# Kernel tuning notes

Measured on AMD Instinct MI355X. Metric: run time of the kernel, lower is better.

The kernel has to match this reference:

```python
import jax, jax.numpy as jnp
import numpy as np

CODEBOOK_SIZE = 512
LATENT_DIM = 12
BATCH = 512
TOKENS = 256


def setup_inputs() -> dict:
    key = jax.random.key(0)
    k1, k2 = jax.random.split(key)
    x = jax.random.normal(k1, (BATCH, TOKENS, LATENT_DIM), dtype=jnp.float32)
    # nn.Embedding init: uniform(-1/K, 1/K)
    lim = 1.0 / CODEBOOK_SIZE
    codebook = jax.random.uniform(k2, (CODEBOOK_SIZE, LATENT_DIM), dtype=jnp.float32,
                                  minval=-lim, maxval=lim)
    return {"x": x, "codebook": codebook}


def reference(x, codebook):
    # same as for torch.cdist (sqrt is monotonic).
    x2 = jnp.sum(x * x, axis=-1, keepdims=True)            # [B, N, 1]
    w2 = jnp.sum(codebook * codebook, axis=-1)             # [K]
    xw = jnp.einsum('bnd,kd->bnk', x, codebook)            # [B, N, K]
    dist2 = x2 - 2.0 * xw + w2                             # [B, N, K]
    indices = jnp.argmin(dist2, axis=-1)                   # [B, N] int
    quantized = codebook[indices]                          # [B, N, D]

    codebook_loss = jnp.mean((quantized - jax.lax.stop_gradient(x)) ** 2)
    commitment_loss = 0.25 * jnp.mean((jax.lax.stop_gradient(quantized) - x) ** 2)
    quantize_loss = codebook_loss + commitment_loss

    # straight-through estimator
    quantized_st = x + jax.lax.stop_gradient(quantized - x)
    return quantized_st, indices, quantize_loss
```

## Files before the change

### kernel.cpp

```cpp
#include <hip/hip_runtime.h>
#include <math.h>

namespace {
constexpr int KCB   = 512;
constexpr int DIM   = 12;
constexpr int NTOK  = 512 * 256;
constexpr int QSIZE = NTOK * DIM;
constexpr int NSPLIT = 8;
constexpr int KCHUNK = KCB / NSPLIT;
constexpr int TPT    = 4;
constexpr int TOKS_PER_BLOCK = 64 * TPT;
constexpr int NBLK   = NTOK / TOKS_PER_BLOCK;
constexpr int WVEC_FLOATS = KCB * DIM;
constexpr int CB_FLOATS   = WVEC_FLOATS + KCB;
constexpr int CB_F4       = CB_FLOATS / 4;
constexpr int SMEM_U64    = 3333;
constexpr int PARTIALS_OFF = 8192;

__global__ __launch_bounds__(256) void pack_cb(const float* __restrict__ cb,
                                               float* __restrict__ ws) {
    int k = blockIdx.x * blockDim.x + threadIdx.x;
    if (k >= KCB) return;
    float w[DIM];
#pragma unroll
    for (int d = 0; d < DIM; ++d) w[d] = cb[k * DIM + d];
    float w2 = 0.f;
#pragma unroll
    for (int d = 0; d < DIM; ++d) w2 += w[d] * w[d];
#pragma unroll
    for (int d = 0; d < DIM; ++d) ws[k * DIM + d] = w[d];
    ws[WVEC_FLOATS + k] = w2;
}

__device__ inline float code_score(const float (&xv)[DIM], float x2,
                                   const float4& c0, const float4& c1,
                                   const float4& c2, float w2k) {
    float xw = 0.f;
    xw = fmaf(xv[0],  c0.x, xw);
    xw = fmaf(xv[1],  c0.y, xw);
    xw = fmaf(xv[2],  c0.z, xw);
    xw = fmaf(xv[3],  c0.w, xw);
    xw = fmaf(xv[4],  c1.x, xw);
    xw = fmaf(xv[5],  c1.y, xw);
    xw = fmaf(xv[6],  c1.z, xw);
    xw = fmaf(xv[7],  c1.w, xw);
    xw = fmaf(xv[8],  c2.x, xw);
    xw = fmaf(xv[9],  c2.y, xw);
    xw = fmaf(xv[10], c2.z, xw);
    xw = fmaf(xv[11], c2.w, xw);
    return fmaf(-2.f, xw, x2) + w2k;
}

__global__ __launch_bounds__(512, 2) void vq_main(const float* __restrict__ x,
                                                  const float* __restrict__ cb,
                                                  const float* __restrict__ pk,
                                                  float* __restrict__ out,
                                                  float* __restrict__ partials) {
    __shared__ unsigned long long smem[SMEM_U64];
    __shared__ float lred[TPT];
    float* lds = (float*)smem;
    const int tid  = threadIdx.x;
    const int lane = tid & 63;
    const int s = __builtin_amdgcn_readfirstlane(tid >> 6);
    const int tbase = blockIdx.x * TOKS_PER_BLOCK;

    {
        float4* l4 = (float4*)lds;
        const float4* g4 = (const float4*)pk;
        for (int i = tid; i < CB_F4; i += 512) l4[i] = g4[i];
    }

    float xs[TPT][DIM];
    float x2[TPT];
#pragma unroll
    for (int j = 0; j < TPT; ++j) {
        const float4* xp = (const float4*)(x + (size_t)(tbase + j * 64 + lane) * DIM);
        float4 a0 = xp[0], a1 = xp[1], a2 = xp[2];
        xs[j][0] = a0.x; xs[j][1] = a0.y; xs[j][2]  = a0.z; xs[j][3]  = a0.w;
        xs[j][4] = a1.x; xs[j][5] = a1.y; xs[j][6]  = a1.z; xs[j][7]  = a1.w;
        xs[j][8] = a2.x; xs[j][9] = a2.y; xs[j][10] = a2.z; xs[j][11] = a2.w;
        float t2 = 0.f;
#pragma unroll
        for (int d = 0; d < DIM; ++d) t2 = fmaf(xs[j][d], xs[j][d], t2);
        x2[j] = t2;
    }

    __syncthreads();

    float best[TPT];
    int   bi[TPT];
#pragma unroll
    for (int j = 0; j < TPT; ++j) { best[j] = INFINITY; bi[j] = 0; }

    const int k0 = s * KCHUNK;
    const float* w2v = lds + WVEC_FLOATS;

    float4 A0, A1, A2; float w2A;
    float4 B0, B1, B2; float w2B;
    {
        const float* c = lds + (size_t)k0 * DIM;
        A0 = *(const float4*)(c + 0);
        A1 = *(const float4*)(c + 4);
        A2 = *(const float4*)(c + 8);
        w2A = w2v[k0];
    }
#pragma unroll 4
    for (int kk = 0; kk < KCHUNK; kk += 2) {
        {
            const float* c = lds + (size_t)(k0 + kk + 1) * DIM;
            B0 = *(const float4*)(c + 0);
            B1 = *(const float4*)(c + 4);
            B2 = *(const float4*)(c + 8);
            w2B = w2v[k0 + kk + 1];
        }
        {
            const int k = k0 + kk;
#pragma unroll
            for (int j = 0; j < TPT; ++j) {
                float d = code_score(xs[j], x2[j], A0, A1, A2, w2A);
                bool c = d < best[j];
                best[j] = c ? d : best[j];
                bi[j]   = c ? k : bi[j];
            }
        }
        {
            const float* c = lds + (size_t)(k0 + kk + 2) * DIM;
            A0 = *(const float4*)(c + 0);
            A1 = *(const float4*)(c + 4);
            A2 = *(const float4*)(c + 8);
            w2A = w2v[k0 + kk + 2];
        }
        {
            const int k = k0 + kk + 1;
#pragma unroll
            for (int j = 0; j < TPT; ++j) {
                float d = code_score(xs[j], x2[j], B0, B1, B2, w2B);
                bool c = d < best[j];
                best[j] = c ? d : best[j];
                bi[j]   = c ? k : bi[j];
            }
        }
    }

    auto mkkey = [](float v, int k) {
        unsigned su = __float_as_uint(v);
        su = (su & 0x80000000u) ? ~su : (su | 0x80000000u);
        return ((unsigned long long)su << 32) | (unsigned)k;
    };
    __syncthreads();
#pragma unroll
    for (int j = 0; j < TPT; ++j)
        smem[s * TOKS_PER_BLOCK + j * 64 + lane] = mkkey(best[j], bi[j]);
    __syncthreads();

    if (s < TPT) {
        const int tok = s * 64 + lane;
        unsigned long long m = smem[tok];
#pragma unroll
        for (int r = 1; r < NSPLIT; ++r) {
            unsigned long long v = smem[r * TOKS_PER_BLOCK + tok];
            m = v < m ? v : m;
        }
        const int bid = (int)(m & 0xffffffffULL);
        unsigned eu = (unsigned)(m >> 32);
        unsigned orig = (eu & 0x80000000u) ? (eu ^ 0x80000000u) : ~eu;
        const float bsc = __uint_as_float(orig);
        const int t = tbase + tok;

        float xv[DIM];
#pragma unroll
        for (int j = 0; j < TPT; ++j)
            if (j == s) {
#pragma unroll
                for (int d = 0; d < DIM; ++d) xv[d] = xs[j][d];
            }

        const float4* wrow = (const float4*)(cb + (size_t)bid * DIM);
        float4 q0 = wrow[0], q1 = wrow[1], q2 = wrow[2];
        float qs[DIM] = {q0.x, q0.y, q0.z, q0.w, q1.x, q1.y, q1.z, q1.w,
                         q2.x, q2.y, q2.z, q2.w};

        float4* qo = (float4*)(out + (size_t)t * DIM);
        float4 r0, r1, r2;
        r0.x = xv[0] + (qs[0] - xv[0]);    r0.y = xv[1] + (qs[1] - xv[1]);
        r0.z = xv[2] + (qs[2] - xv[2]);    r0.w = xv[3] + (qs[3] - xv[3]);
        r1.x = xv[4] + (qs[4] - xv[4]);    r1.y = xv[5] + (qs[5] - xv[5]);
        r1.z = xv[6] + (qs[6] - xv[6]);    r1.w = xv[7] + (qs[7] - xv[7]);
        r2.x = xv[8] + (qs[8] - xv[8]);    r2.y = xv[9] + (qs[9] - xv[9]);
        r2.z = xv[10] + (qs[10] - xv[10]); r2.w = xv[11] + (qs[11] - xv[11]);
        qo[0] = r0; qo[1] = r1; qo[2] = r2;

        out[QSIZE + t] = (float)bid;

        float ls = bsc * (1.25f / (float)QSIZE);
#pragma unroll
        for (int off = 32; off > 0; off >>= 1) ls += __shfl_down(ls, off);
        if (lane == 0) lred[s] = ls;
    }
    __syncthreads();
    if (tid == 0)
        partials[blockIdx.x] = (lred[0] + lred[1]) + (lred[2] + lred[3]);
}

__global__ __launch_bounds__(512) void reduce_loss(const float* __restrict__ partials,
                                                   float* __restrict__ out) {
    __shared__ float r[8];
    float v = partials[threadIdx.x];
#pragma unroll
    for (int off = 32; off > 0; off >>= 1) v += __shfl_down(v, off);
    if ((threadIdx.x & 63) == 0) r[threadIdx.x >> 6] = v;
    __syncthreads();
    if (threadIdx.x == 0) {
        float t = 0.f;
#pragma unroll
        for (int i = 0; i < 8; ++i) t += r[i];
        out[QSIZE + NTOK] = t;
    }
}
}

extern "C" void kernel_launch(void* const* d_in, const int* in_sizes, int n_in,
                              void* d_out, int out_size, void* d_ws, size_t ws_size,
                              hipStream_t stream) {
    const float* x  = (const float*)d_in[0];
    const float* cb = (const float*)d_in[1];
    float* out = (float*)d_out;
    float* pk  = (float*)d_ws;
    float* partials = (float*)d_ws + PARTIALS_OFF;

    pack_cb<<<2, 256, 0, stream>>>(cb, pk);
    vq_main<<<NBLK, 512, 0, stream>>>(x, cb, pk, out, partials);
    reduce_loss<<<1, 512, 0, stream>>>(partials, out);
}
```

Measured before the change: 94.52 us.

## Split codebook across blocks and move emission to a separate kernel

The scan kernel now handles half the codebook per block, doubling the grid to 1024 blocks, and computes codebook norms in LDS instead of in a separate pack kernel. Each block writes per-token min keys to workspace, and a new emit kernel merges the two halves, writes outputs, and accumulates the loss with atomicAdd. This targets low occupancy and tail effects from only 512 blocks and removes two tiny launches. In exchange it adds global traffic for the keys and a second read of x, and the atomic loss sum makes its float rounding order nondeterministic.

```diff
diff --git a/kernel.cpp b/kernel.cpp
--- a/kernel.cpp
+++ b/kernel.cpp
@@ -7,30 +7,17 @@
 constexpr int NTOK  = 512 * 256;
 constexpr int QSIZE = NTOK * DIM;
 constexpr int NSPLIT = 8;
-constexpr int KCHUNK = KCB / NSPLIT;
+constexpr int KHALF  = 2;
+constexpr int KCODES = KCB / KHALF;
+constexpr int KCHUNK = KCODES / NSPLIT;
 constexpr int TPT    = 4;
 constexpr int TOKS_PER_BLOCK = 64 * TPT;
-constexpr int NBLK   = NTOK / TOKS_PER_BLOCK;
-constexpr int WVEC_FLOATS = KCB * DIM;
-constexpr int CB_FLOATS   = WVEC_FLOATS + KCB;
-constexpr int CB_F4       = CB_FLOATS / 4;
-constexpr int SMEM_U64    = 3333;
-constexpr int PARTIALS_OFF = 8192;
-
-__global__ __launch_bounds__(256) void pack_cb(const float* __restrict__ cb,
-                                               float* __restrict__ ws) {
-    int k = blockIdx.x * blockDim.x + threadIdx.x;
-    if (k >= KCB) return;
-    float w[DIM];
-#pragma unroll
-    for (int d = 0; d < DIM; ++d) w[d] = cb[k * DIM + d];
-    float w2 = 0.f;
-#pragma unroll
-    for (int d = 0; d < DIM; ++d) w2 += w[d] * w[d];
-#pragma unroll
-    for (int d = 0; d < DIM; ++d) ws[k * DIM + d] = w[d];
-    ws[WVEC_FLOATS + k] = w2;
-}
+constexpr int NTG    = NTOK / TOKS_PER_BLOCK;
+constexpr int NBLK1  = NTG * KHALF;
+constexpr int WVEC   = KCODES * DIM;
+constexpr int SMEM_U64 = NSPLIT * TOKS_PER_BLOCK;
+constexpr int EMIT_THREADS = 256;
+constexpr int NBLK2 = NTOK / EMIT_THREADS;
 
 __device__ inline float code_score(const float (&xv)[DIM], float x2,
                                    const float4& c0, const float4& c1,
@@ -51,23 +38,32 @@
     return fmaf(-2.f, xw, x2) + w2k;
 }
 
-__global__ __launch_bounds__(512, 2) void vq_main(const float* __restrict__ x,
+__device__ inline unsigned long long mkkey(float v, int k) {
+    unsigned su = __float_as_uint(v);
+    su = (su & 0x80000000u) ? ~su : (su | 0x80000000u);
+    return ((unsigned long long)su << 32) | (unsigned)k;
+}
+
+__global__ __launch_bounds__(512, 6) void vq_scan(const float* __restrict__ x,
                                                   const float* __restrict__ cb,
-                                                  const float* __restrict__ pk,
-                                                  float* __restrict__ out,
-                                                  float* __restrict__ partials) {
+                                                  unsigned long long* __restrict__ keys,
+                                                  float* __restrict__ out) {
     __shared__ unsigned long long smem[SMEM_U64];
-    __shared__ float lred[TPT];
     float* lds = (float*)smem;
     const int tid  = threadIdx.x;
     const int lane = tid & 63;
     const int s = __builtin_amdgcn_readfirstlane(tid >> 6);
-    const int tbase = blockIdx.x * TOKS_PER_BLOCK;
+    const int tg = blockIdx.x & (NTG - 1);
+    const int kh = blockIdx.x >> 9;
+    const int kbase = kh * KCODES;
+    const int tbase = tg * TOKS_PER_BLOCK;
+
+    if (blockIdx.x == 0 && tid == 0) out[QSIZE + NTOK] = 0.f;
 
     {
+        const float4* g4 = (const float4*)(cb + (size_t)kbase * DIM);
         float4* l4 = (float4*)lds;
-        const float4* g4 = (const float4*)pk;
-        for (int i = tid; i < CB_F4; i += 512) l4[i] = g4[i];
+        for (int i = tid; i < WVEC / 4; i += 512) l4[i] = g4[i];
     }
 
     float xs[TPT][DIM];
@@ -87,34 +83,44 @@
 
     __syncthreads();
 
+    if (tid < KCODES) {
+        const float* w = lds + (size_t)tid * DIM;
+        float w2 = 0.f;
+#pragma unroll
+        for (int d = 0; d < DIM; ++d) w2 = fmaf(w[d], w[d], w2);
+        lds[WVEC + tid] = w2;
+    }
+    __syncthreads();
+
     float best[TPT];
     int   bi[TPT];
 #pragma unroll
     for (int j = 0; j < TPT; ++j) { best[j] = INFINITY; bi[j] = 0; }
 
-    const int k0 = s * KCHUNK;
-    const float* w2v = lds + WVEC_FLOATS;
+    const int k0l = s * KCHUNK;
+    const int gk0 = kbase + k0l;
+    const float* w2v = lds + WVEC;
 
     float4 A0, A1, A2; float w2A;
     float4 B0, B1, B2; float w2B;
     {
-        const float* c = lds + (size_t)k0 * DIM;
+        const float* c = lds + (size_t)k0l * DIM;
         A0 = *(const float4*)(c + 0);
         A1 = *(const float4*)(c + 4);
         A2 = *(const float4*)(c + 8);
-        w2A = w2v[k0];
+        w2A = w2v[k0l];
     }
 #pragma unroll 4
     for (int kk = 0; kk < KCHUNK; kk += 2) {
         {
-            const float* c = lds + (size_t)(k0 + kk + 1) * DIM;
+            const float* c = lds + (size_t)(k0l + kk + 1) * DIM;
             B0 = *(const float4*)(c + 0);
             B1 = *(const float4*)(c + 4);
             B2 = *(const float4*)(c + 8);
-            w2B = w2v[k0 + kk + 1];
-        }
-        {
-            const int k = k0 + kk;
+            w2B = w2v[k0l + kk + 1];
+        }
+        {
+            const int k = gk0 + kk;
 #pragma unroll
             for (int j = 0; j < TPT; ++j) {
                 float d = code_score(xs[j], x2[j], A0, A1, A2, w2A);
@@ -124,14 +130,14 @@
             }
         }
         {
-            const float* c = lds + (size_t)(k0 + kk + 2) * DIM;
+            const float* c = lds + (size_t)(k0l + kk + 2) * DIM;
             A0 = *(const float4*)(c + 0);
             A1 = *(const float4*)(c + 4);
             A2 = *(const float4*)(c + 8);
-            w2A = w2v[k0 + kk + 2];
-        }
-        {
-            const int k = k0 + kk + 1;
+            w2A = w2v[k0l + kk + 2];
+        }
+        {
+            const int k = gk0 + kk + 1;
 #pragma unroll
             for (int j = 0; j < TPT; ++j) {
                 float d = code_score(xs[j], x2[j], B0, B1, B2, w2B);
@@ -142,11 +148,6 @@
         }
     }
 
-    auto mkkey = [](float v, int k) {
-        unsigned su = __float_as_uint(v);
-        su = (su & 0x80000000u) ? ~su : (su | 0x80000000u);
-        return ((unsigned long long)su << 32) | (unsigned)k;
-    };
     __syncthreads();
 #pragma unroll
     for (int j = 0; j < TPT; ++j)
@@ -161,60 +162,56 @@
             unsigned long long v = smem[r * TOKS_PER_BLOCK + tok];
             m = v < m ? v : m;
         }
-        const int bid = (int)(m & 0xffffffffULL);
-        unsigned eu = (unsigned)(m >> 32);
-        unsigned orig = (eu & 0x80000000u) ? (eu ^ 0x80000000u) : ~eu;
-        const float bsc = __uint_as_float(orig);
-        const int t = tbase + tok;
-
-        float xv[DIM];
-#pragma unroll
-        for (int j = 0; j < TPT; ++j)
-            if (j == s) {
-#pragma unroll
-                for (int d = 0; d < DIM; ++d) xv[d] = xs[j][d];
-            }
-
-        const float4* wrow = (const float4*)(cb + (size_t)bid * DIM);
-        float4 q0 = wrow[0], q1 = wrow[1], q2 = wrow[2];
-        float qs[DIM] = {q0.x, q0.y, q0.z, q0.w, q1.x, q1.y, q1.z, q1.w,
-                         q2.x, q2.y, q2.z, q2.w};
-
-        float4* qo = (float4*)(out + (size_t)t * DIM);
-        float4 r0, r1, r2;
-        r0.x = xv[0] + (qs[0] - xv[0]);    r0.y = xv[1] + (qs[1] - xv[1]);
-        r0.z = xv[2] + (qs[2] - xv[2]);    r0.w = xv[3] + (qs[3] - xv[3]);
-        r1.x = xv[4] + (qs[4] - xv[4]);    r1.y = xv[5] + (qs[5] - xv[5]);
-        r1.z = xv[6] + (qs[6] - xv[6]);    r1.w = xv[7] + (qs[7] - xv[7]);
-        r2.x = xv[8] + (qs[8] - xv[8]);    r2.y = xv[9] + (qs[9] - xv[9]);
-        r2.z = xv[10] + (qs[10] - xv[10]); r2.w = xv[11] + (qs[11] - xv[11]);
-        qo[0] = r0; qo[1] = r1; qo[2] = r2;
-
-        out[QSIZE + t] = (float)bid;
-
-        float ls = bsc * (1.25f / (float)QSIZE);
-#pragma unroll
-        for (int off = 32; off > 0; off >>= 1) ls += __shfl_down(ls, off);
-        if (lane == 0) lred[s] = ls;
-    }
-    __syncthreads();
-    if (tid == 0)
-        partials[blockIdx.x] = (lred[0] + lred[1]) + (lred[2] + lred[3]);
-}
-
-__global__ __launch_bounds__(512) void reduce_loss(const float* __restrict__ partials,
-                                                   float* __restrict__ out) {
-    __shared__ float r[8];
-    float v = partials[threadIdx.x];
-#pragma unroll
-    for (int off = 32; off > 0; off >>= 1) v += __shfl_down(v, off);
-    if ((threadIdx.x & 63) == 0) r[threadIdx.x >> 6] = v;
+        keys[(size_t)kh * NTOK + tbase + tok] = m;
+    }
+}
+
+__global__ __launch_bounds__(EMIT_THREADS) void vq_emit(const float* __restrict__ x,
+                                                        const float* __restrict__ cb,
+                                                        const unsigned long long* __restrict__ keys,
+                                                        float* __restrict__ out) {
+    __shared__ float lred[EMIT_THREADS / 64];
+    const int t = blockIdx.x * EMIT_THREADS + threadIdx.x;
+
+    unsigned long long m0 = keys[t];
+    unsigned long long m1 = keys[(size_t)NTOK + t];
+    unsigned long long m = m1 < m0 ? m1 : m0;
+
+    const int bid = (int)(m & 0xffffffffULL);
+    unsigned eu = (unsigned)(m >> 32);
+    unsigned orig = (eu & 0x80000000u) ? (eu ^ 0x80000000u) : ~eu;
+    const float bsc = __uint_as_float(orig);
+
+    const float4* xp = (const float4*)(x + (size_t)t * DIM);
+    float4 a0 = xp[0], a1 = xp[1], a2 = xp[2];
+    float xv[DIM] = {a0.x, a0.y, a0.z, a0.w, a1.x, a1.y, a1.z, a1.w,
+                     a2.x, a2.y, a2.z, a2.w};
+
+    const float4* wrow = (const float4*)(cb + (size_t)bid * DIM);
+    float4 q0 = wrow[0], q1 = wrow[1], q2 = wrow[2];
+    float qs[DIM] = {q0.x, q0.y, q0.z, q0.w, q1.x, q1.y, q1.z, q1.w,
+                     q2.x, q2.y, q2.z, q2.w};
+
+    float4* qo = (float4*)(out + (size_t)t * DIM);
+    float4 r0, r1, r2;
+    r0.x = xv[0] + (qs[0] - xv[0]);    r0.y = xv[1] + (qs[1] - xv[1]);
+    r0.z = xv[2] + (qs[2] - xv[2]);    r0.w = xv[3] + (qs[3] - xv[3]);
+    r1.x = xv[4] + (qs[4] - xv[4]);    r1.y = xv[5] + (qs[5] - xv[5]);
+    r1.z = xv[6] + (qs[6] - xv[6]);    r1.w = xv[7] + (qs[7] - xv[7]);
+    r2.x = xv[8] + (qs[8] - xv[8]);    r2.y = xv[9] + (qs[9] - xv[9]);
+    r2.z = xv[10] + (qs[10] - xv[10]); r2.w = xv[11] + (qs[11] - xv[11]);
+    qo[0] = r0; qo[1] = r1; qo[2] = r2;
+
+    out[QSIZE + t] = (float)bid;
+
+    float ls = bsc * (1.25f / (float)QSIZE);
+#pragma unroll
+    for (int off = 32; off > 0; off >>= 1) ls += __shfl_down(ls, off);
+    if ((threadIdx.x & 63) == 0) lred[threadIdx.x >> 6] = ls;
     __syncthreads();
     if (threadIdx.x == 0) {
-        float t = 0.f;
-#pragma unroll
-        for (int i = 0; i < 8; ++i) t += r[i];
-        out[QSIZE + NTOK] = t;
+        float v = (lred[0] + lred[1]) + (lred[2] + lred[3]);
+        atomicAdd(out + QSIZE + NTOK, v);
     }
 }
 }
@@ -225,10 +222,8 @@
     const float* x  = (const float*)d_in[0];
     const float* cb = (const float*)d_in[1];
     float* out = (float*)d_out;
-    float* pk  = (float*)d_ws;
-    float* partials = (float*)d_ws + PARTIALS_OFF;
-
-    pack_cb<<<2, 256, 0, stream>>>(cb, pk);
-    vq_main<<<NBLK, 512, 0, stream>>>(x, cb, pk, out, partials);
-    reduce_loss<<<1, 512, 0, stream>>>(partials, out);
-}
+    unsigned long long* keys = (unsigned long long*)d_ws;
+
+    vq_scan<<<NBLK1, 512, 0, stream>>>(x, cb, keys, out);
+    vq_emit<<<NBLK2, EMIT_THREADS, 0, stream>>>(x, cb, keys, out);
+}
```

New measurement: 252.8 us. 168% more time.

## Read padded codebook via scalar global loads and fold loss reduction into atomics

Applied to the files above, without the earlier changes.

Drops the per-block copy of the codebook into LDS. Each wave now reads a 16-float padded row layout (vector plus its squared norm) straight from global memory; the row address is wave-uniform, so the compiler can use scalar loads. Tokens per thread fall from 4 to 2, which doubles the block count, and occupancy is raised to 4 blocks per CU. The final reduce kernel is replaced by one atomicAdd per block into an output slot that pack_cb zeroes first. The trade-offs are more redundant codebook reads per block and a float-atomic sum whose order is not deterministic.

```diff
diff --git a/kernel.cpp b/kernel.cpp
--- a/kernel.cpp
+++ b/kernel.cpp
@@ -8,29 +8,10 @@
 constexpr int QSIZE = NTOK * DIM;
 constexpr int NSPLIT = 8;
 constexpr int KCHUNK = KCB / NSPLIT;
-constexpr int TPT    = 4;
+constexpr int TPT    = 2;
 constexpr int TOKS_PER_BLOCK = 64 * TPT;
 constexpr int NBLK   = NTOK / TOKS_PER_BLOCK;
-constexpr int WVEC_FLOATS = KCB * DIM;
-constexpr int CB_FLOATS   = WVEC_FLOATS + KCB;
-constexpr int CB_F4       = CB_FLOATS / 4;
-constexpr int SMEM_U64    = 3333;
-constexpr int PARTIALS_OFF = 8192;
-
-__global__ __launch_bounds__(256) void pack_cb(const float* __restrict__ cb,
-                                               float* __restrict__ ws) {
-    int k = blockIdx.x * blockDim.x + threadIdx.x;
-    if (k >= KCB) return;
-    float w[DIM];
-#pragma unroll
-    for (int d = 0; d < DIM; ++d) w[d] = cb[k * DIM + d];
-    float w2 = 0.f;
-#pragma unroll
-    for (int d = 0; d < DIM; ++d) w2 += w[d] * w[d];
-#pragma unroll
-    for (int d = 0; d < DIM; ++d) ws[k * DIM + d] = w[d];
-    ws[WVEC_FLOATS + k] = w2;
-}
+constexpr int ROWF   = 16;
 
 __device__ inline float code_score(const float (&xv)[DIM], float x2,
                                    const float4& c0, const float4& c1,
@@ -51,24 +32,44 @@
     return fmaf(-2.f, xw, x2) + w2k;
 }
 
-__global__ __launch_bounds__(512, 2) void vq_main(const float* __restrict__ x,
+__device__ inline unsigned long long mkkey(float v, int k) {
+    unsigned su = __float_as_uint(v);
+    su = (su & 0x80000000u) ? ~su : (su | 0x80000000u);
+    return ((unsigned long long)su << 32) | (unsigned)k;
+}
+
+__global__ __launch_bounds__(256) void pack_cb(const float* __restrict__ cb,
+                                               float* __restrict__ pk,
+                                               float* __restrict__ out) {
+    int k = blockIdx.x * blockDim.x + threadIdx.x;
+    if (k == 0) out[QSIZE + NTOK] = 0.f;
+    if (k >= KCB) return;
+    float w[DIM];
+#pragma unroll
+    for (int d = 0; d < DIM; ++d) w[d] = cb[k * DIM + d];
+    float w2 = 0.f;
+#pragma unroll
+    for (int d = 0; d < DIM; ++d) w2 = fmaf(w[d], w[d], w2);
+#pragma unroll
+    for (int d = 0; d < DIM; ++d) pk[k * ROWF + d] = w[d];
+    pk[k * ROWF + 12] = w2;
+    pk[k * ROWF + 13] = 0.f; pk[k * ROWF + 14] = 0.f; pk[k * ROWF + 15] = 0.f;
+    if (k == KCB - 1) {
+#pragma unroll
+        for (int d = 0; d < ROWF; ++d) pk[KCB * ROWF + d] = 0.f;
+    }
+}
+
+__global__ __launch_bounds__(512, 4) void vq_main(const float* __restrict__ x,
                                                   const float* __restrict__ cb,
                                                   const float* __restrict__ pk,
-                                                  float* __restrict__ out,
-                                                  float* __restrict__ partials) {
-    __shared__ unsigned long long smem[SMEM_U64];
+                                                  float* __restrict__ out) {
+    __shared__ unsigned long long keys[NSPLIT * TOKS_PER_BLOCK];
     __shared__ float lred[TPT];
-    float* lds = (float*)smem;
     const int tid  = threadIdx.x;
     const int lane = tid & 63;
     const int s = __builtin_amdgcn_readfirstlane(tid >> 6);
     const int tbase = blockIdx.x * TOKS_PER_BLOCK;
-
-    {
-        float4* l4 = (float4*)lds;
-        const float4* g4 = (const float4*)pk;
-        for (int i = tid; i < CB_F4; i += 512) l4[i] = g4[i];
-    }
 
     float xs[TPT][DIM];
     float x2[TPT];
@@ -85,33 +86,28 @@
         x2[j] = t2;
     }
 
-    __syncthreads();
-
     float best[TPT];
     int   bi[TPT];
 #pragma unroll
     for (int j = 0; j < TPT; ++j) { best[j] = INFINITY; bi[j] = 0; }
 
     const int k0 = s * KCHUNK;
-    const float* w2v = lds + WVEC_FLOATS;
+    const float* cw = pk + (size_t)k0 * ROWF;
 
     float4 A0, A1, A2; float w2A;
     float4 B0, B1, B2; float w2B;
-    {
-        const float* c = lds + (size_t)k0 * DIM;
-        A0 = *(const float4*)(c + 0);
-        A1 = *(const float4*)(c + 4);
-        A2 = *(const float4*)(c + 8);
-        w2A = w2v[k0];
-    }
-#pragma unroll 4
+    A0 = *(const float4*)(cw + 0);
+    A1 = *(const float4*)(cw + 4);
+    A2 = *(const float4*)(cw + 8);
+    w2A = cw[12];
+#pragma unroll 2
     for (int kk = 0; kk < KCHUNK; kk += 2) {
         {
-            const float* c = lds + (size_t)(k0 + kk + 1) * DIM;
+            const float* c = cw + (size_t)(kk + 1) * ROWF;
             B0 = *(const float4*)(c + 0);
             B1 = *(const float4*)(c + 4);
             B2 = *(const float4*)(c + 8);
-            w2B = w2v[k0 + kk + 1];
+            w2B = c[12];
         }
         {
             const int k = k0 + kk;
@@ -124,11 +120,11 @@
             }
         }
         {
-            const float* c = lds + (size_t)(k0 + kk + 2) * DIM;
+            const float* c = cw + (size_t)(kk + 2) * ROWF;
             A0 = *(const float4*)(c + 0);
             A1 = *(const float4*)(c + 4);
             A2 = *(const float4*)(c + 8);
-            w2A = w2v[k0 + kk + 2];
+            w2A = c[12];
         }
         {
             const int k = k0 + kk + 1;
@@ -142,23 +138,17 @@
         }
     }
 
-    auto mkkey = [](float v, int k) {
-        unsigned su = __float_as_uint(v);
-        su = (su & 0x80000000u) ? ~su : (su | 0x80000000u);
-        return ((unsigned long long)su << 32) | (unsigned)k;
-    };
-    __syncthreads();
 #pragma unroll
     for (int j = 0; j < TPT; ++j)
-        smem[s * TOKS_PER_BLOCK + j * 64 + lane] = mkkey(best[j], bi[j]);
+        keys[s * TOKS_PER_BLOCK + j * 64 + lane] = mkkey(best[j], bi[j]);
     __syncthreads();
 
     if (s < TPT) {
         const int tok = s * 64 + lane;
-        unsigned long long m = smem[tok];
+        unsigned long long m = keys[tok];
 #pragma unroll
         for (int r = 1; r < NSPLIT; ++r) {
-            unsigned long long v = smem[r * TOKS_PER_BLOCK + tok];
+            unsigned long long v = keys[r * TOKS_PER_BLOCK + tok];
             m = v < m ? v : m;
         }
         const int bid = (int)(m & 0xffffffffULL);
@@ -198,24 +188,7 @@
         if (lane == 0) lred[s] = ls;
     }
     __syncthreads();
-    if (tid == 0)
-        partials[blockIdx.x] = (lred[0] + lred[1]) + (lred[2] + lred[3]);
-}
-
-__global__ __launch_bounds__(512) void reduce_loss(const float* __restrict__ partials,
-                                                   float* __restrict__ out) {
-    __shared__ float r[8];
-    float v = partials[threadIdx.x];
-#pragma unroll
-    for (int off = 32; off > 0; off >>= 1) v += __shfl_down(v, off);
-    if ((threadIdx.x & 63) == 0) r[threadIdx.x >> 6] = v;
-    __syncthreads();
-    if (threadIdx.x == 0) {
-        float t = 0.f;
-#pragma unroll
-        for (int i = 0; i < 8; ++i) t += r[i];
-        out[QSIZE + NTOK] = t;
-    }
+    if (tid == 0) atomicAdd(out + QSIZE + NTOK, lred[0] + lred[1]);
 }
 }
 
@@ -226,9 +199,7 @@
     const float* cb = (const float*)d_in[1];
     float* out = (float*)d_out;
     float* pk  = (float*)d_ws;
-    float* partials = (float*)d_ws + PARTIALS_OFF;
-
-    pack_cb<<<2, 256, 0, stream>>>(cb, pk);
-    vq_main<<<NBLK, 512, 0, stream>>>(x, cb, pk, out, partials);
-    reduce_loss<<<1, 512, 0, stream>>>(partials, out);
-}
+
+    pack_cb<<<2, 256, 0, stream>>>(cb, pk, out);
+    vq_main<<<NBLK, 512, 0, stream>>>(x, cb, pk, out);
+}
```

After: 88.85 us. 1.06x faster.
